# Kernel tuning notes

Measured on AMD Instinct MI355X. Metric: run time of the kernel, lower is better.

The kernel has to match this reference:

```python
import jax, jax.numpy as jnp
import numpy as np

P = 12           # AR order == number of rollout steps
N = 2048         # input_size (nodes)
B = 128          # batch
C = 1            # channels (only channel 0 used)


def setup_inputs() -> dict:
    key = jax.random.key(0)
    kx, kw = jax.random.split(key)
    x = jax.random.normal(kx, (B, N, C, P), dtype=jnp.float32)
    W = jax.random.normal(kw, (P, N, N), dtype=jnp.float32)
    return {"x": x, "W": W}


def reference(x, W):
    # x: [B, N, C, L]; take channel 0 and transpose -> [B, L(=p), N]
    xt = jnp.transpose(x[:, :, 0, :], (0, 2, 1))

    def step(xc, _):
        # einsum('ijk,bik->bij') followed by sum over i fuses to 'ijk,bik->bj'
        y = jnp.einsum('ijk,bik->bj', W, xc)              # [B, N]
        xc = jnp.concatenate([xc[:, 1:, :], y[:, None, :]], axis=1)  # shift window
        return xc, y

    _, ys = jax.lax.scan(step, xt, None, length=12)       # ys: [12, B, N]
    return jnp.transpose(ys, (1, 2, 0))                   # [B, N, 12]
```

## Files before the change

### kernel.cpp

```cpp
#include <hip/hip_runtime.h>
#include <hip/hip_bf16.h>
#include <stdint.h>


typedef _Float16 f16x8 __attribute__((ext_vector_type(8)));
typedef float    f32x4 __attribute__((ext_vector_type(4)));

#define B_ 128
#define N_ 2048
#define P_ 12
#define K_ (P_*N_)
#define KSPLIT 48
#define KCH (K_/KSPLIT)
#define NPHASE (KCH/64)
#define NTILES 16
#define NKP (K_/64)

#define WPK_BYTES   ((size_t)NTILES*NKP*16384)
#define H_SLOT_BYTES ((size_t)B_*N_*2)
#define H_BYTES     (23*H_SLOT_BYTES)
#define PART_BYTES  ((size_t)KSPLIT*B_*N_*4)
#define WS_NEEDED   (WPK_BYTES + H_BYTES + PART_BYTES)

__device__ __constant__ int E_TAB[11] = {7, 13, 18, 24, 29, 35, 40, 46, 51, 57, 62};

__device__ __forceinline__ int e_of_slot(int g) {
    return (g < 12) ? 0 : E_TAB[g - 12];
}
__device__ __forceinline__ float pow2f(int e) {
    return __uint_as_float((uint32_t)(127 + e) << 23);
}

union F16x8 { _Float16 h[8]; uint4 q; };
union F16x4 { _Float16 h[4]; uint2 q; };

__device__ __forceinline__ uint32_t h_off(int slot, int b, int k) {
    return (uint32_t)slot * (uint32_t)H_SLOT_BYTES
         + (uint32_t)(k >> 5) * 8192u + (uint32_t)(((k >> 3) & 3) << 11)
         + (uint32_t)(b << 4) + (uint32_t)((k & 7) << 1);
}

__device__ __forceinline__ size_t w_tile_base(int nt, int pk) {
    return ((size_t)nt * NKP + (size_t)pk) * 16384;
}

__global__ void prep_w(const float* __restrict__ W, char* __restrict__ Wp) {
    __shared__ float tile[128][68];
    int id = blockIdx.x;
    int nt = id / NKP, pk = id % NKP;
    int i = pk >> 5;
    int k0 = (pk & 31) << 6;
    int j0 = nt << 7;
    int t = threadIdx.x;
    #pragma unroll
    for (int pass = 0; pass < 8; ++pass) {
        int jl = pass * 16 + (t >> 4);
        int kq = (t & 15) * 4;
        float4 v = *(const float4*)(W + ((size_t)i * N_ + (j0 + jl)) * N_ + k0 + kq);
        tile[jl][kq + 0] = v.x; tile[jl][kq + 1] = v.y;
        tile[jl][kq + 2] = v.z; tile[jl][kq + 3] = v.w;
    }
    __syncthreads();
    int ksub = t >> 7, c = t & 127;
    char* base = Wp + w_tile_base(nt, pk) + (ksub << 13);
    #pragma unroll
    for (int ko = 0; ko < 4; ++ko) {
        F16x8 o;
        #pragma unroll
        for (int q = 0; q < 8; ++q) o.h[q] = (_Float16)tile[c][ksub * 32 + ko * 8 + q];
        uint32_t off = (uint32_t)((c << 6) + (ko << 4)) ^ (uint32_t)((c & 7) << 4);
        *(uint4*)(base + off) = o.q;
    }
}

__global__ void prep_x(const float* __restrict__ x, char* __restrict__ H) {
    int tid = blockIdx.x * 256 + threadIdx.x;
    int b = tid >> 8;
    int n0 = (tid & 255) << 3;
    const float4* s4 = (const float4*)(x + ((size_t)b * N_ + n0) * P_);
    float4 tmp[24];
    #pragma unroll
    for (int i2 = 0; i2 < 24; ++i2) tmp[i2] = s4[i2];
    #pragma unroll
    for (int p = 0; p < 12; ++p) {
        F16x8 o;
        #pragma unroll
        for (int q = 0; q < 8; ++q) {
            int fi = q * 12 + p;
            float4 blk = tmp[fi >> 2];
            float f = ((fi & 3) == 0) ? blk.x : ((fi & 3) == 1) ? blk.y : ((fi & 3) == 2) ? blk.z : blk.w;
            o.h[q] = (_Float16)f;
        }
        *(uint4*)(H + h_off(p, b, n0)) = o.q;
    }
}

__global__ __launch_bounds__(256, 3) void gemm_step(
        const char* __restrict__ Wp, const char* __restrict__ H,
        float* __restrict__ partial, int st)
{
    __shared__ alignas(16) char ldsB[2][16384];
    const int tid  = threadIdx.x;
    const int lane = tid & 63;
    const int wv   = tid >> 6;
    const int wr   = wv >> 1;
    const int wc   = wv & 1;
    const int bid  = blockIdx.x;
    const int ks    = bid % KSPLIT;
    const int ntile = bid / KSPLIT;
    const int jbase = (ntile << 7) + (wc << 6) + (lane & 15);
    const int ko   = lane >> 4;
    const int kbase = ks * KCH;
    const int pk0  = kbase >> 6;

    uint32_t boff[4];
    #pragma unroll
    for (int nf = 0; nf < 4; ++nf) {
        int c = (wc << 6) + (nf << 4) + (lane & 15);
        boff[nf] = (uint32_t)((c << 6) + (ko << 4)) ^ (uint32_t)((c & 7) << 4);
    }

    auto stage = [&](int buf, int ph) {
        const char* src = Wp + w_tile_base(ntile, pk0 + ph);
        #pragma unroll
        for (int j = 0; j < 4; ++j) {
            uint32_t o = (uint32_t)(j << 12) + (uint32_t)(tid << 4);
            __builtin_amdgcn_global_load_lds(
                (const __attribute__((address_space(1))) void*)(src + o),
                (__attribute__((address_space(3))) void*)&ldsB[buf][(j << 12) + (wv << 10)], 16, 0, 0);
        }
    };
    auto loadA = [&](int ph, f16x8 a[2][4]) {
        #pragma unroll
        for (int ksub = 0; ksub < 2; ++ksub) {
            int kg = kbase + (ph << 6) + (ksub << 5);
            const char* sb = H + (size_t)(st + (kg >> 11)) * H_SLOT_BYTES
                           + (uint32_t)(((kg & 2047) >> 5) << 13) + (uint32_t)(ko << 11);
            #pragma unroll
            for (int m = 0; m < 4; ++m) {
                int brow = (wr << 6) + (m << 4) + (lane & 15);
                a[ksub][m] = *(const f16x8*)(sb + (brow << 4));
            }
        }
    };

    f32x4 acc[4][4];
    #pragma unroll
    for (int m = 0; m < 4; ++m)
        #pragma unroll
        for (int n = 0; n < 4; ++n) acc[m][n] = (f32x4){0.f, 0.f, 0.f, 0.f};

    f16x8 a[2][4];
    loadA(0, a);
    stage(0, 0);
    __syncthreads();

    for (int ph = 0; ph < NPHASE; ++ph) {
        if (ph + 1 < NPHASE) stage((ph & 1) ^ 1, ph + 1);
        const char* lb = &ldsB[ph & 1][0];
        f16x8 bf[2][4];
        #pragma unroll
        for (int ksub = 0; ksub < 2; ++ksub)
            #pragma unroll
            for (int nf = 0; nf < 4; ++nf)
                bf[ksub][nf] = *(const f16x8*)(lb + (ksub << 13) + boff[nf]);
        f16x8 an[2][4];
        if (ph + 1 < NPHASE) loadA(ph + 1, an);
        #pragma unroll
        for (int ksub = 0; ksub < 2; ++ksub)
            #pragma unroll
            for (int m = 0; m < 4; ++m)
                #pragma unroll
                for (int nf = 0; nf < 4; ++nf)
                    acc[m][nf] = __builtin_amdgcn_mfma_f32_16x16x32_f16(a[ksub][m], bf[ksub][nf], acc[m][nf], 0, 0, 0);
        #pragma unroll
        for (int ksub = 0; ksub < 2; ++ksub)
            #pragma unroll
            for (int m = 0; m < 4; ++m) a[ksub][m] = an[ksub][m];
        __syncthreads();
    }

    const int r0 = (lane >> 4) << 2;
    float* pb = partial + ((size_t)ks * B_ + (wr << 6) + r0) * N_ + jbase;
    #pragma unroll
    for (int m = 0; m < 4; ++m)
        #pragma unroll
        for (int n = 0; n < 4; ++n)
            #pragma unroll
            for (int r = 0; r < 4; ++r)
                pb[(size_t)(m * 16 + r) * N_ + n * 16] = acc[m][n][r];
}

__global__ void reduce_step(const float* __restrict__ partial, float* __restrict__ out,
                            char* __restrict__ H, int t)
{
    int tid = blockIdx.x * 256 + threadIdx.x;
    int b = tid >> 9;
    int n0 = (tid & 511) << 2;
    float s0 = 0.f, s1 = 0.f, s2 = 0.f, s3 = 0.f;
    #pragma unroll 4
    for (int ksI = 0; ksI < KSPLIT; ++ksI) {
        float sc = pow2f(e_of_slot(t + (ksI >> 2)));
        float4 a = *(const float4*)(partial + ((size_t)ksI * B_ + b) * N_ + n0);
        s0 += a.x * sc; s1 += a.y * sc; s2 += a.z * sc; s3 += a.w * sc;
    }
    float* ob = out + ((size_t)b * N_ + n0) * P_ + t;
    ob[0 * P_] = s0; ob[1 * P_] = s1; ob[2 * P_] = s2; ob[3 * P_] = s3;
    if (t < 11) {
        float ds = pow2f(-E_TAB[t]);
        F16x4 o;
        o.h[0] = (_Float16)(s0 * ds); o.h[1] = (_Float16)(s1 * ds);
        o.h[2] = (_Float16)(s2 * ds); o.h[3] = (_Float16)(s3 * ds);
        *(uint2*)(H + h_off(12 + t, b, n0)) = o.q;
    }
}

__global__ void naive_step(const float* __restrict__ x, const float* __restrict__ W,
                           float* __restrict__ out, int t)
{
    int tid = blockIdx.x * 256 + threadIdx.x;
    int b = tid >> 11;
    int j = tid & (N_ - 1);
    float acc = 0.f;
    for (int i = 0; i < 12; ++i) {
        int g = t + i;
        const float* src = (g < 12) ? (x   + (size_t)b * (N_ * 12) + g)
                                    : (out + (size_t)b * (N_ * 12) + (g - 12));
        const float* wr = W + ((size_t)i * N_ + j) * N_;
        for (int k = 0; k < N_; ++k)
            acc += wr[k] * src[(size_t)k * 12];
    }
    out[((size_t)b * N_ + j) * 12 + t] = acc;
}

extern "C" void kernel_launch(void* const* d_in, const int* in_sizes, int n_in,
                              void* d_out, int out_size, void* d_ws, size_t ws_size,
                              hipStream_t stream)
{
    const float* x = (const float*)d_in[0];
    const float* W = (const float*)d_in[1];
    float* out = (float*)d_out;

    if (ws_size < WS_NEEDED) {
        for (int t = 0; t < 12; ++t)
            naive_step<<<1024, 256, 0, stream>>>(x, W, out, t);
        return;
    }

    char* ws = (char*)d_ws;
    char* Wp = ws;
    char* H  = Wp + WPK_BYTES;
    float* partial = (float*)(H + H_BYTES);

    prep_w<<<6144, 256, 0, stream>>>(W, Wp);
    prep_x<<<128, 256, 0, stream>>>(x, H);
    for (int t = 0; t < 12; ++t) {
        gemm_step<<<768, 256, 0, stream>>>(Wp, H, partial, t);
        reduce_step<<<256, 256, 0, stream>>>(partial, out, H, t);
    }
}
```

Baseline: 508.4 us.

## Store split-K partials in fp16 with in-kernel exponent rescaling, reduce split count

Measured after the change: 451.7 us. 11.2% less time.

```diff
diff --git a/kernel.cpp b/kernel.cpp
--- a/kernel.cpp
+++ b/kernel.cpp
@@ -1,5 +1,4 @@
 #include <hip/hip_runtime.h>
-#include <hip/hip_bf16.h>
 #include <stdint.h>
 
 
@@ -10,7 +9,7 @@
 #define N_ 2048
 #define P_ 12
 #define K_ (P_*N_)
-#define KSPLIT 48
+#define KSPLIT 32
 #define KCH (K_/KSPLIT)
 #define NPHASE (KCH/64)
 #define NTILES 16
@@ -19,7 +18,7 @@
 #define WPK_BYTES   ((size_t)NTILES*NKP*16384)
 #define H_SLOT_BYTES ((size_t)B_*N_*2)
 #define H_BYTES     (23*H_SLOT_BYTES)
-#define PART_BYTES  ((size_t)KSPLIT*B_*N_*4)
+#define PART_BYTES  ((size_t)KSPLIT*B_*N_*2)
 #define WS_NEEDED   (WPK_BYTES + H_BYTES + PART_BYTES)
 
 __device__ __constant__ int E_TAB[11] = {7, 13, 18, 24, 29, 35, 40, 46, 51, 57, 62};
@@ -32,7 +31,7 @@
 }
 
 union F16x8 { _Float16 h[8]; uint4 q; };
-union F16x4 { _Float16 h[4]; uint2 q; };
+union F16x4v { _Float16 h[4]; uint2 q; };
 
 __device__ __forceinline__ uint32_t h_off(int slot, int b, int k) {
     return (uint32_t)slot * (uint32_t)H_SLOT_BYTES
@@ -95,9 +94,9 @@
     }
 }
 
-__global__ __launch_bounds__(256, 3) void gemm_step(
+__global__ __launch_bounds__(256, 2) void gemm_step(
         const char* __restrict__ Wp, const char* __restrict__ H,
-        float* __restrict__ partial, int st)
+        _Float16* __restrict__ partial, int st)
 {
     __shared__ alignas(16) char ldsB[2][16384];
     const int tid  = threadIdx.x;
@@ -155,7 +154,17 @@
     stage(0, 0);
     __syncthreads();
 
+    int cur_e = e_of_slot(st + (kbase >> 11));
     for (int ph = 0; ph < NPHASE; ++ph) {
+        int e_new = e_of_slot(st + ((kbase + (ph << 6)) >> 11));
+        if (e_new != cur_e) {
+            float f = pow2f(cur_e - e_new);
+            #pragma unroll
+            for (int m = 0; m < 4; ++m)
+                #pragma unroll
+                for (int n = 0; n < 4; ++n) acc[m][n] *= f;
+            cur_e = e_new;
+        }
         if (ph + 1 < NPHASE) stage((ph & 1) ^ 1, ph + 1);
         const char* lb = &ldsB[ph & 1][0];
         f16x8 bf[2][4];
@@ -181,17 +190,17 @@
     }
 
     const int r0 = (lane >> 4) << 2;
-    float* pb = partial + ((size_t)ks * B_ + (wr << 6) + r0) * N_ + jbase;
+    _Float16* pb = partial + ((size_t)ks * B_ + (wr << 6) + r0) * N_ + jbase;
     #pragma unroll
     for (int m = 0; m < 4; ++m)
         #pragma unroll
         for (int n = 0; n < 4; ++n)
             #pragma unroll
             for (int r = 0; r < 4; ++r)
-                pb[(size_t)(m * 16 + r) * N_ + n * 16] = acc[m][n][r];
-}
-
-__global__ void reduce_step(const float* __restrict__ partial, float* __restrict__ out,
+                pb[(size_t)(m * 16 + r) * N_ + n * 16] = (_Float16)acc[m][n][r];
+}
+
+__global__ void reduce_step(const _Float16* __restrict__ partial, float* __restrict__ out,
                             char* __restrict__ H, int t)
 {
     int tid = blockIdx.x * 256 + threadIdx.x;
@@ -199,16 +208,18 @@
     int n0 = (tid & 511) << 2;
     float s0 = 0.f, s1 = 0.f, s2 = 0.f, s3 = 0.f;
     #pragma unroll 4
-    for (int ksI = 0; ksI < KSPLIT; ++ksI) {
-        float sc = pow2f(e_of_slot(t + (ksI >> 2)));
-        float4 a = *(const float4*)(partial + ((size_t)ksI * B_ + b) * N_ + n0);
-        s0 += a.x * sc; s1 += a.y * sc; s2 += a.z * sc; s3 += a.w * sc;
+    for (int c = 0; c < KSPLIT; ++c) {
+        float sc = pow2f(e_of_slot(t + ((c * KCH + (KCH - 64)) >> 11)));
+        F16x4v p;
+        p.q = *(const uint2*)(partial + ((size_t)c * B_ + b) * N_ + n0);
+        s0 += (float)p.h[0] * sc; s1 += (float)p.h[1] * sc;
+        s2 += (float)p.h[2] * sc; s3 += (float)p.h[3] * sc;
     }
     float* ob = out + ((size_t)b * N_ + n0) * P_ + t;
     ob[0 * P_] = s0; ob[1 * P_] = s1; ob[2 * P_] = s2; ob[3 * P_] = s3;
     if (t < 11) {
         float ds = pow2f(-E_TAB[t]);
-        F16x4 o;
+        F16x4v o;
         o.h[0] = (_Float16)(s0 * ds); o.h[1] = (_Float16)(s1 * ds);
         o.h[2] = (_Float16)(s2 * ds); o.h[3] = (_Float16)(s3 * ds);
         *(uint2*)(H + h_off(12 + t, b, n0)) = o.q;
@@ -250,12 +261,12 @@
     char* ws = (char*)d_ws;
     char* Wp = ws;
     char* H  = Wp + WPK_BYTES;
-    float* partial = (float*)(H + H_BYTES);
+    _Float16* partial = (_Float16*)(H + H_BYTES);
 
     prep_w<<<6144, 256, 0, stream>>>(W, Wp);
     prep_x<<<128, 256, 0, stream>>>(x, H);
     for (int t = 0; t < 12; ++t) {
-        gemm_step<<<768, 256, 0, stream>>>(Wp, H, partial, t);
+        gemm_step<<<512, 256, 0, stream>>>(Wp, H, partial, t);
         reduce_step<<<256, 256, 0, stream>>>(partial, out, H, t);
     }
 }
```
